# Kernel tuning notes

Hardware: AMD Instinct MI355X
Metric: run time of the kernel (lower is better)

## Reference

```python
import jax, jax.numpy as jnp
import numpy as np
from jax import lax

# Mamba2 block (training path: mamba_split_conv1d_scan_combined equivalent)
B = 2; L = 2048; D_MODEL = 2048
INTER = 4096          # ssm_intermediate_size
NH = 64; HD = INTER // NH   # num_heads, head_dim
N = 128               # ssm_state_size
G = 1                 # n_groups
K = 4                 # conv kernel
CS = 256              # chunk size
EPS = 1e-5
CONV_DIM = INTER + 2 * G * N          # 4352
PROJ_DIM = INTER + CONV_DIM + NH      # 8512


def setup_inputs() -> dict:
    key = jax.random.key(0)
    ks = jax.random.split(key, 4)
    std = 0.02
    return {
        "hidden_states": jax.random.normal(ks[0], (B, L, D_MODEL), jnp.float32),
        "W_in": jax.random.normal(ks[1], (PROJ_DIM, D_MODEL), jnp.float32) * std,
        "conv_w": jax.random.normal(ks[2], (CONV_DIM, K), jnp.float32) * std,
        "conv_b": jnp.zeros((CONV_DIM,), jnp.float32),
        "dt_bias": jnp.ones((NH,), jnp.float32),
        "A_log": jnp.log(jnp.arange(1, NH + 1, dtype=jnp.float32)),
        "D": jnp.ones((NH,), jnp.float32),
        "norm_w": jnp.ones((INTER,), jnp.float32),
        "W_out": jax.random.normal(ks[3], (D_MODEL, INTER), jnp.float32) * std,
    }


def _segsum(x):
    # x: [..., s] -> [..., s, s] lower-triangular cumulative sums (masked with -inf)
    s = x.shape[-1]
    xc = jnp.cumsum(x, axis=-1)
    d = xc[..., :, None] - xc[..., None, :]
    return jnp.where(jnp.tril(jnp.ones((s, s), dtype=bool)), d, -jnp.inf)


def _forward(hidden_states, W_in, conv_w, conv_b, dt_bias, A_log, D, norm_w, W_out):
    proj = hidden_states @ W_in.T                              # [B,L,PROJ_DIM]
    gate = proj[..., :INTER]
    hBC = proj[..., INTER:INTER + CONV_DIM]
    dt = proj[..., INTER + CONV_DIM:]                          # [B,L,NH]

    # causal depthwise conv1d + silu
    xc = hBC.transpose(0, 2, 1)                                # [B,CONV_DIM,L]
    y = lax.conv_general_dilated(
        xc, conv_w[:, None, :], (1,), [(K - 1, 0)],
        dimension_numbers=("NCH", "OIH", "NCH"), feature_group_count=CONV_DIM)
    hBC = jax.nn.silu(y + conv_b[None, :, None]).transpose(0, 2, 1)

    x = hBC[..., :INTER].reshape(B, L, NH, HD)
    Bm = hBC[..., INTER:INTER + G * N].reshape(B, L, G, N)
    Cm = hBC[..., INTER + G * N:].reshape(B, L, G, N)

    dtv = jax.nn.softplus(dt + dt_bias)                        # [B,L,NH], dt_softplus=True
    A = -jnp.exp(A_log)                                        # [NH]

    # ---- chunked selective scan (SSD) ----
    c = L // CS
    xch = x.reshape(B, c, CS, NH, HD)
    dtch = dtv.reshape(B, c, CS, NH)
    Bh = jnp.repeat(Bm.reshape(B, c, CS, G, N), NH // G, axis=3)   # [B,c,s,NH,N]
    Ch = jnp.repeat(Cm.reshape(B, c, CS, G, N), NH // G, axis=3)

    dA = (dtch * A).transpose(0, 3, 1, 2)                      # [B,NH,c,s]
    Acum = jnp.cumsum(dA, axis=-1)                             # [B,NH,c,s]
    Lmat = jnp.exp(_segsum(dA))                                # [B,NH,c,s,s]

    # within-chunk (diagonal block) output
    Ydiag = jnp.einsum("bcihn,bcjhn,bhcij,bcjh,bcjhp->bcihp",
                       Ch, Bh, Lmat, dtch, xch)

    # per-chunk states
    decay_states = jnp.exp(Acum[..., -1:] - Acum)              # [B,NH,c,s]
    states = jnp.einsum("bcjhn,bhcj,bcjh,bcjhp->bchpn",
                        Bh, decay_states, dtch, xch)           # [B,c,NH,HD,N]

    # inter-chunk recurrence (scan over chunks)
    chunk_decay = jnp.exp(Acum[..., -1])                       # [B,NH,c]

    def step(carry, inp):
        st, dec = inp
        new = dec[:, :, None, None] * carry + st
        return new, carry                                      # emit state at chunk start

    init = jnp.zeros((B, NH, HD, N), dtype=x.dtype)
    _, prev = lax.scan(step, init,
                       (states.transpose(1, 0, 2, 3, 4), chunk_decay.transpose(2, 0, 1)))
    prev = prev.transpose(1, 0, 2, 3, 4)                       # [B,c,NH,HD,N]

    Yoff = jnp.einsum("bcihn,bchpn,bhci->bcihp", Ch, prev, jnp.exp(Acum))

    Y = (Ydiag + Yoff).reshape(B, L, NH, HD) + x * D[None, None, :, None]
    yout = Y.reshape(B, L, INTER)

    # gated RMSNorm (norm_before_gate=False): gate first, then normalize
    yout = yout * jax.nn.silu(gate)
    yout = yout * lax.rsqrt(jnp.mean(yout * yout, axis=-1, keepdims=True) + EPS) * norm_w
    return yout @ W_out.T                                      # [B,L,D_MODEL]


def reference(hidden_states, W_in, conv_w, conv_b, dt_bias, A_log, D, norm_w, W_out):
    return _forward(hidden_states, W_in, conv_w, conv_b, dt_bias, A_log, D, norm_w, W_out)
```

## Files before the change

kernel.cpp:

```cpp
#include <hip/hip_runtime.h>
#include <cstdint>

typedef __bf16 bf16;
typedef __bf16 bf16x8 __attribute__((ext_vector_type(8)));
typedef __bf16 bf16x4 __attribute__((ext_vector_type(4)));
typedef float  f32x4  __attribute__((ext_vector_type(4)));

#define BQ     2
#define LQ     2048
#define DMODEL 2048
#define INTER  4096
#define NH     64
#define HD     64
#define NS     128
#define CS     256
#define NC     8
#define CONVD  4352
#define PROJD  8512
#define PROJP  8576
#define MTOT   4096
#define EPSF   1e-5f
#define LOG2E  1.44269504088896f

__device__ __forceinline__ void async_ld16(const bf16* g, bf16* l) {
  __builtin_amdgcn_global_load_lds(
      (__attribute__((address_space(1))) void*)(uintptr_t)g,
      (__attribute__((address_space(3))) void*)l, 16, 0, 0);
}

__device__ __forceinline__ float siluf(float x) { return x / (1.f + expf(-x)); }

__global__ void cast4_k(const float* __restrict__ in, bf16* __restrict__ out, long n4) {
  long i = (long)blockIdx.x * 256 + threadIdx.x;
  if (i >= n4) return;
  float4 v = ((const float4*)in)[i];
  bf16x4 o; o[0] = (bf16)v.x; o[1] = (bf16)v.y; o[2] = (bf16)v.z; o[3] = (bf16)v.w;
  ((bf16x4*)out)[i] = o;
}

__global__ void cast_pad_win_k(const float* __restrict__ W, bf16* __restrict__ out) {
  long i = (long)blockIdx.x * 256 + threadIdx.x;
  long tot = (long)PROJP * (DMODEL / 4);
  if (i >= tot) return;
  long row = i / (DMODEL / 4);
  long k4  = i % (DMODEL / 4);
  bf16x4 o;
  if (row < PROJD) {
    float4 v = ((const float4*)W)[row * (DMODEL / 4) + k4];
    o[0] = (bf16)v.x; o[1] = (bf16)v.y; o[2] = (bf16)v.z; o[3] = (bf16)v.w;
  } else {
    o[0] = o[1] = o[2] = o[3] = (bf16)0.f;
  }
  ((bf16x4*)out)[i] = o;
}

#define BM 128
#define BN 128
#define BK 32

__global__ __launch_bounds__(256) void gemm_bt(
    const bf16* __restrict__ A, const bf16* __restrict__ W,
    bf16* __restrict__ Cb, float* __restrict__ Cf,
    int M, int Nn, int K, int outf32)
{
  __shared__ bf16 As[BM * BK];
  __shared__ bf16 Bs[BN * BK];
  const int tid  = threadIdx.x;
  const int wave = tid >> 6;
  const int lane = tid & 63;
  const long tm = (long)blockIdx.y * BM;
  const long tn = (long)blockIdx.x * BN;
  const int wm = (wave >> 1) * 64;
  const int wn = (wave & 1) * 64;
  const int quad = lane >> 4;
  const int r16  = lane & 15;

  f32x4 acc[4][4] = {};

  for (long k0 = 0; k0 < K; k0 += BK) {
    __syncthreads();
    #pragma unroll
    for (int p = 0; p < 2; ++p) {
      int row = p * 64 + (tid >> 2);
      int kc  = (tid & 3) * 8;
      async_ld16(A + (tm + row) * K + k0 + kc, &As[(p * 256 + wave * 64) * 8]);
      async_ld16(W + (tn + row) * K + k0 + kc, &Bs[(p * 256 + wave * 64) * 8]);
    }
    __syncthreads();
    bf16x8 af[4], bfr[4];
    #pragma unroll
    for (int i = 0; i < 4; ++i)
      af[i] = *(const bf16x8*)&As[(wm + i * 16 + r16) * BK + quad * 8];
    #pragma unroll
    for (int j = 0; j < 4; ++j)
      bfr[j] = *(const bf16x8*)&Bs[(wn + j * 16 + r16) * BK + quad * 8];
    #pragma unroll
    for (int i = 0; i < 4; ++i)
      #pragma unroll
      for (int j = 0; j < 4; ++j)
        acc[i][j] = __builtin_amdgcn_mfma_f32_16x16x32_bf16(af[i], bfr[j], acc[i][j], 0, 0, 0);
  }

  #pragma unroll
  for (int i = 0; i < 4; ++i)
    #pragma unroll
    for (int j = 0; j < 4; ++j) {
      long r0 = tm + wm + i * 16 + quad * 4;
      long cc = tn + wn + j * 16 + r16;
      #pragma unroll
      for (int reg = 0; reg < 4; ++reg) {
        long idx = (r0 + reg) * (long)Nn + cc;
        if (outf32) Cf[idx] = acc[i][j][reg];
        else        Cb[idx] = (bf16)acc[i][j][reg];
      }
    }
}

__global__ void conv_silu_k(const bf16* __restrict__ proj,
                            const float* __restrict__ conv_w,
                            const float* __restrict__ conv_b,
                            bf16* __restrict__ xconv,
                            bf16* __restrict__ Bmb, bf16* __restrict__ Cmb)
{
  int ch = blockIdx.x * 256 + threadIdx.x;
  if (ch >= CONVD) return;
  long bl = blockIdx.y;
  int l = (int)(bl & (LQ - 1));
  float acc = conv_b[ch];
  #pragma unroll
  for (int t = 0; t < 4; ++t) {
    int ls = l - 3 + t;
    if (ls >= 0)
      acc += (float)proj[(bl - 3 + t) * PROJP + INTER + ch] * conv_w[ch * 4 + t];
  }
  float y = siluf(acc);
  if (ch < INTER)            xconv[bl * INTER + ch] = (bf16)y;
  else if (ch < INTER + NS)  Bmb[bl * NS + (ch - INTER)] = (bf16)y;
  else                       Cmb[bl * NS + (ch - INTER - NS)] = (bf16)y;
}

__global__ __launch_bounds__(CS) void dt_prep_k(
    const bf16* __restrict__ proj, const float* __restrict__ dt_bias,
    const float* __restrict__ A_log,
    float* __restrict__ dtv, float* __restrict__ acum, float* __restrict__ cdec)
{
  int bx = blockIdx.x;
  int ci = bx & 7;
  int bh = bx >> 3;
  int h  = bh & 63;
  int b  = bh >> 6;
  int i  = threadIdx.x;
  long pos = (long)b * LQ + ci * CS + i;
  float draw = (float)proj[pos * PROJP + INTER + CONVD + h] + dt_bias[h];
  float dv = draw > 20.f ? draw : log1pf(expf(draw));
  float Ah = -expf(A_log[h]);
  __shared__ float s[CS];
  s[i] = dv * Ah;
  __syncthreads();
  for (int off = 1; off < CS; off <<= 1) {
    float t = (i >= off) ? s[i - off] : 0.f;
    __syncthreads();
    s[i] += t;
    __syncthreads();
  }
  long base = (long)bx * CS;
  dtv[base + i]  = dv;
  acum[base + i] = s[i];
  if (i == 0) cdec[bx] = expf(s[CS - 1]);
}

__global__ __launch_bounds__(256) void gmat_k(
    const bf16* __restrict__ Cmb, const bf16* __restrict__ Bmb, float* __restrict__ Gnt)
{
  int q  = blockIdx.x;
  int bc = blockIdx.y;
  long bl0 = (long)(bc >> 3) * LQ + (bc & 7) * CS;
  int wave = threadIdx.x >> 6, lane = threadIdx.x & 63;
  int quad = lane >> 4, r16 = lane & 15;
  int i0 = (q >> 1) * 128 + (wave >> 1) * 64;
  int j0 = (q & 1)  * 128 + (wave & 1)  * 64;

  f32x4 acc[4][4] = {};
  #pragma unroll
  for (int kt = 0; kt < 4; ++kt) {
    int k0 = kt * 32 + quad * 8;
    bf16x8 af[4], bfv[4];
    #pragma unroll
    for (int it = 0; it < 4; ++it)
      af[it] = *(const bf16x8*)&Cmb[(bl0 + i0 + it * 16 + r16) * NS + k0];
    #pragma unroll
    for (int nt = 0; nt < 4; ++nt)
      bfv[nt] = *(const bf16x8*)&Bmb[(bl0 + j0 + nt * 16 + r16) * NS + k0];
    #pragma unroll
    for (int it = 0; it < 4; ++it)
      #pragma unroll
      for (int nt = 0; nt < 4; ++nt)
        acc[it][nt] = __builtin_amdgcn_mfma_f32_16x16x32_bf16(af[it], bfv[nt], acc[it][nt], 0, 0, 0);
  }
  #pragma unroll
  for (int it = 0; it < 4; ++it)
    #pragma unroll
    for (int nt = 0; nt < 4; ++nt)
      #pragma unroll
      for (int reg = 0; reg < 4; ++reg) {
        int i = i0 + it * 16 + quad * 4 + reg;
        int j = j0 + nt * 16 + r16;
        Gnt[((long)bc * CS + i) * CS + j] = acc[it][nt][reg];
      }
}

__global__ __launch_bounds__(256) void states_k(
    const bf16* __restrict__ xconv, const bf16* __restrict__ Bmb,
    const float* __restrict__ dtv, const float* __restrict__ acum,
    bf16* __restrict__ states)
{
  int bx = blockIdx.x;
  int h = bx & 63, bc = bx >> 6;
  int b = bc >> 3, ci = bc & 7;
  long bl0 = (long)b * LQ + ci * CS;
  long abase = ((long)(b * NH + h) * NC + ci) * CS;
  int t = threadIdx.x;
  __shared__ float ac_s[CS];
  __shared__ float ws_s[CS];
  __shared__ float xw[64][64];
  __shared__ float Bl[64][NS];
  ac_s[t] = acum[abase + t];
  __syncthreads();
  float alast = ac_s[CS - 1];
  ws_s[t] = expf(alast - ac_s[t]) * dtv[abase + t];
  int p = t & 63, nb = t >> 6;
  float accv[32] = {};
  for (int jt = 0; jt < 4; ++jt) {
    __syncthreads();
    for (int r = 0; r < 16; ++r) {
      int jj = (t >> 6) + r * 4;
      xw[jj][p] = (float)xconv[(bl0 + jt * 64 + jj) * INTER + h * HD + p] * ws_s[jt * 64 + jj];
    }
    for (int r = 0; r < 32; ++r) {
      int idx = t + r * 256;
      int jj = idx >> 7, n = idx & 127;
      Bl[jj][n] = (float)Bmb[(bl0 + jt * 64 + jj) * NS + n];
    }
    __syncthreads();
    for (int jj = 0; jj < 64; ++jj) {
      float xv = xw[jj][p];
      #pragma unroll
      for (int n0 = 0; n0 < 32; ++n0)
        accv[n0] += xv * Bl[jj][nb * 32 + n0];
    }
  }
  long sb = ((long)bx * HD + p) * NS + nb * 32;
  #pragma unroll
  for (int n0 = 0; n0 < 32; ++n0) states[sb + n0] = (bf16)accv[n0];
}

__global__ void scan_k(bf16* __restrict__ st, const float* __restrict__ cdec)
{
  long t = (long)blockIdx.x * 256 + threadIdx.x;
  int n = (int)(t & 127);
  int p = (int)((t >> 7) & 63);
  int h = (int)((t >> 13) & 63);
  int b = (int)(t >> 19);
  float carry = 0.f;
  for (int ci = 0; ci < NC; ++ci) {
    long idx = (((long)(b * NC + ci) * NH + h) * HD + p) * NS + n;
    float v = (float)st[idx];
    st[idx] = (bf16)carry;
    carry = cdec[(b * NH + h) * NC + ci] * carry + v;
  }
}

#define XTP 392
__global__ __launch_bounds__(256) void ymix_k(
    const bf16* __restrict__ xconv, const float* __restrict__ Gnt,
    const bf16* __restrict__ prev, const bf16* __restrict__ Cmb,
    const float* __restrict__ dtv, const float* __restrict__ acum,
    const float* __restrict__ Dp, bf16* __restrict__ Y)
{
  int bx = blockIdx.x;
  int h = bx & 63, bc = bx >> 6;
  int b = bc >> 3, ci = bc & 7;
  long bl0 = (long)b * LQ + ci * CS;
  long abase = ((long)(b * NH + h) * NC + ci) * CS;
  int t = threadIdx.x;
  int wave = t >> 6, lane = t & 63;
  int quad = lane >> 4, r16 = lane & 15;
  int iw = wave * 64;

  __shared__ bf16 Xt[64][XTP];
  __shared__ float a2s[CS], dts[CS], eas[CS];

  {
    float ac = acum[abase + t];
    a2s[t] = ac * LOG2E;
    dts[t] = dtv[abase + t];
    eas[t] = expf(ac);
  }
  {
    int col = t & 63, grp = t >> 6;
    for (int r = 0; r < 64; ++r) {
      int j = grp * 64 + r;
      Xt[col][j] = xconv[(bl0 + j) * INTER + h * HD + col];
    }
  }
  for (int r = 0; r < 32; ++r) {
    int idx = t + r * 256;
    int n = idx & 127, p = idx >> 7;
    Xt[p][256 + n] = prev[((long)bx * HD + p) * NS + n];
  }
  __syncthreads();

  f32x4 acc[4][4] = {};

  for (int kt = 0; kt < 12; ++kt) {
    int k0 = kt * 32;
    bool cpart = (k0 >= 256);
    if (!cpart && k0 > iw + 63) continue;

    bf16x8 bfrag[4];
    #pragma unroll
    for (int nt = 0; nt < 4; ++nt)
      bfrag[nt] = *(const bf16x8*)&Xt[nt * 16 + r16][k0 + quad * 8];

    if (!cpart) {
      int j0 = k0 + quad * 8;
      float dt8[8], a28[8];
      *(float4*)&dt8[0] = *(const float4*)&dts[j0];
      *(float4*)&dt8[4] = *(const float4*)&dts[j0 + 4];
      *(float4*)&a28[0] = *(const float4*)&a2s[j0];
      *(float4*)&a28[4] = *(const float4*)&a2s[j0 + 4];
      #pragma unroll
      for (int it = 0; it < 4; ++it) {
        if (k0 > iw + it * 16 + 15) continue;
        int i = iw + it * 16 + r16;
        float a2i = a2s[i];
        const float* gp = &Gnt[((long)bc * CS + i) * CS + j0];
        float g[8];
        *(float4*)&g[0] = *(const float4*)gp;
        *(float4*)&g[4] = *(const float4*)(gp + 4);
        bf16x8 af;
        #pragma unroll
        for (int jj = 0; jj < 8; ++jj) {
          float v = g[jj] * dt8[jj] * exp2f(a2i - a28[jj]);
          v = (j0 + jj <= i) ? v : 0.f;
          af[jj] = (bf16)v;
        }
        #pragma unroll
        for (int nt = 0; nt < 4; ++nt)
          acc[it][nt] = __builtin_amdgcn_mfma_f32_16x16x32_bf16(af, bfrag[nt], acc[it][nt], 0, 0, 0);
      }
    } else {
      int n0 = k0 - 256 + quad * 8;
      #pragma unroll
      for (int it = 0; it < 4; ++it) {
        int i = iw + it * 16 + r16;
        float e = eas[i];
        bf16x8 cv = *(const bf16x8*)&Cmb[(bl0 + i) * NS + n0];
        bf16x8 af;
        #pragma unroll
        for (int jj = 0; jj < 8; ++jj)
          af[jj] = (bf16)(e * (float)cv[jj]);
        #pragma unroll
        for (int nt = 0; nt < 4; ++nt)
          acc[it][nt] = __builtin_amdgcn_mfma_f32_16x16x32_bf16(af, bfrag[nt], acc[it][nt], 0, 0, 0);
      }
    }
  }

  float Dh = Dp[h];
  #pragma unroll
  for (int it = 0; it < 4; ++it)
    #pragma unroll
    for (int nt = 0; nt < 4; ++nt) {
      int i0 = iw + it * 16 + quad * 4;
      int p  = nt * 16 + r16;
      bf16x4 xv = *(const bf16x4*)&Xt[p][i0];
      #pragma unroll
      for (int reg = 0; reg < 4; ++reg) {
        float v = acc[it][nt][reg] + Dh * (float)xv[reg];
        Y[(bl0 + i0 + reg) * INTER + h * HD + p] = (bf16)v;
      }
    }
}

__global__ __launch_bounds__(256) void norm_k(
    bf16* __restrict__ Y, const bf16* __restrict__ proj,
    const float* __restrict__ norm_w)
{
  long bl = blockIdx.x;
  int t = threadIdx.x;
  __shared__ float yb[INTER];
  __shared__ float red[256];
  float ss = 0.f;
  for (int r = 0; r < 16; ++r) {
    int ch = t + r * 256;
    float g = (float)proj[bl * PROJP + ch];
    float yv = (float)Y[bl * INTER + ch] * siluf(g);
    yb[ch] = yv;
    ss += yv * yv;
  }
  red[t] = ss;
  __syncthreads();
  for (int s = 128; s > 0; s >>= 1) {
    if (t < s) red[t] += red[t + s];
    __syncthreads();
  }
  float scale = rsqrtf(red[0] / (float)INTER + EPSF);
  for (int r = 0; r < 16; ++r) {
    int ch = t + r * 256;
    Y[bl * INTER + ch] = (bf16)(yb[ch] * scale * norm_w[ch]);
  }
}

extern "C" void kernel_launch(void* const* d_in, const int* in_sizes, int n_in,
                              void* d_out, int out_size, void* d_ws, size_t ws_size,
                              hipStream_t stream)
{
  (void)in_sizes; (void)n_in; (void)out_size; (void)ws_size;
  const float* hidden  = (const float*)d_in[0];
  const float* W_in    = (const float*)d_in[1];
  const float* conv_w  = (const float*)d_in[2];
  const float* conv_b  = (const float*)d_in[3];
  const float* dt_bias = (const float*)d_in[4];
  const float* A_log   = (const float*)d_in[5];
  const float* Dp      = (const float*)d_in[6];
  const float* norm_w  = (const float*)d_in[7];
  const float* W_out   = (const float*)d_in[8];
  float* out = (float*)d_out;

  char* ws    = (char*)d_ws;
  bf16* projb = (bf16*)(ws);
  char* base2 = ws + 70254592;
  bf16*  hb    = (bf16*)(base2);
  bf16*  winb  = (bf16*)(base2 + 16777216);
  bf16*  xconv = (bf16*)(base2);
  bf16*  st    = (bf16*)(base2 + 33554432);
  float* Gnt   = (float*)(base2 + 50331648);
  bf16*  Bmb   = (bf16*)(base2 + 54525952);
  bf16*  Cmb   = (bf16*)(base2 + 55574528);
  float* dtv   = (float*)(base2 + 56623104);
  float* acum  = (float*)(base2 + 57671680);
  float* cdec  = (float*)(base2 + 58720256);
  bf16*  Yb    = xconv;
  bf16*  woutb = st;

  cast4_k<<<dim3((unsigned)((MTOT * (long)DMODEL / 4 + 255) / 256)), 256, 0, stream>>>(
      hidden, hb, (long)MTOT * DMODEL / 4);
  cast_pad_win_k<<<dim3((unsigned)(((long)PROJP * (DMODEL / 4) + 255) / 256)), 256, 0, stream>>>(
      W_in, winb);
  gemm_bt<<<dim3(PROJP / BN, MTOT / BM), 256, 0, stream>>>(
      hb, winb, projb, nullptr, MTOT, PROJP, DMODEL, 0);

  conv_silu_k<<<dim3(CONVD / 256, MTOT), 256, 0, stream>>>(
      projb, conv_w, conv_b, xconv, Bmb, Cmb);
  dt_prep_k<<<dim3(BQ * NH * NC), CS, 0, stream>>>(
      projb, dt_bias, A_log, dtv, acum, cdec);
  gmat_k<<<dim3(4, BQ * NC), 256, 0, stream>>>(Cmb, Bmb, Gnt);
  states_k<<<dim3(BQ * NC * NH), 256, 0, stream>>>(xconv, Bmb, dtv, acum, st);
  scan_k<<<dim3(BQ * NH * HD * NS / 256), 256, 0, stream>>>(st, cdec);
  ymix_k<<<dim3(BQ * NC * NH), 256, 0, stream>>>(
      xconv, Gnt, st, Cmb, dtv, acum, Dp, Yb);

  cast4_k<<<dim3((unsigned)((DMODEL * (long)INTER / 4 + 255) / 256)), 256, 0, stream>>>(
      W_out, woutb, (long)DMODEL * INTER / 4);
  norm_k<<<dim3(MTOT), 256, 0, stream>>>(Yb, projb, norm_w);
  gemm_bt<<<dim3(DMODEL / BN, MTOT / BM), 256, 0, stream>>>(
      Yb, woutb, nullptr, out, MTOT, DMODEL, INTER, 1);
}
```

Baseline: 802.4 us.

## Use MFMA for chunk state computation and swizzle GEMM block order

The per-chunk states kernel now uses bf16 MFMA instructions in place of scalar FP32 FMAs. To supply the B operand in k-contiguous form, the conv kernel also writes a per-chunk transposed copy of B, and x is staged transposed in LDS with the decay weights applied before the bf16 cast. The GEMM additionally remaps block indices into groups of 8 row tiles to improve L2 reuse. The tradeoffs are extra strided global writes for the B transpose and some extra rounding from casting the weighted x to bf16.

```diff
diff --git a/kernel.cpp b/kernel.cpp
--- a/kernel.cpp
+++ b/kernel.cpp
@@ -68,8 +68,19 @@
   const int tid  = threadIdx.x;
   const int wave = tid >> 6;
   const int lane = tid & 63;
-  const long tm = (long)blockIdx.y * BM;
-  const long tn = (long)blockIdx.x * BN;
+
+  int bxi, byi;
+  {
+    int b = blockIdx.y * gridDim.x + blockIdx.x;
+    if ((gridDim.y & 7) == 0) {
+      int gs = gridDim.x * 8;
+      int g = b / gs, r = b % gs;
+      byi = g * 8 + (r & 7);
+      bxi = r >> 3;
+    } else { bxi = blockIdx.x; byi = blockIdx.y; }
+  }
+  const long tm = (long)byi * BM;
+  const long tn = (long)bxi * BN;
   const int wm = (wave >> 1) * 64;
   const int wn = (wave & 1) * 64;
   const int quad = lane >> 4;
@@ -120,7 +131,8 @@
                             const float* __restrict__ conv_w,
                             const float* __restrict__ conv_b,
                             bf16* __restrict__ xconv,
-                            bf16* __restrict__ Bmb, bf16* __restrict__ Cmb)
+                            bf16* __restrict__ Bmb, bf16* __restrict__ Cmb,
+                            bf16* __restrict__ Bt)
 {
   int ch = blockIdx.x * 256 + threadIdx.x;
   if (ch >= CONVD) return;
@@ -134,9 +146,16 @@
       acc += (float)proj[(bl - 3 + t) * PROJP + INTER + ch] * conv_w[ch * 4 + t];
   }
   float y = siluf(acc);
-  if (ch < INTER)            xconv[bl * INTER + ch] = (bf16)y;
-  else if (ch < INTER + NS)  Bmb[bl * NS + (ch - INTER)] = (bf16)y;
-  else                       Cmb[bl * NS + (ch - INTER - NS)] = (bf16)y;
+  if (ch < INTER) {
+    xconv[bl * INTER + ch] = (bf16)y;
+  } else if (ch < INTER + NS) {
+    int n = ch - INTER;
+    Bmb[bl * NS + n] = (bf16)y;
+    int b = (int)(bl >> 11), ci = l >> 8, j = l & 255;
+    Bt[(((long)(b * NC + ci) * NS) + n) * CS + j] = (bf16)y;
+  } else {
+    Cmb[bl * NS + (ch - INTER - NS)] = (bf16)y;
+  }
 }
 
 __global__ __launch_bounds__(CS) void dt_prep_k(
@@ -210,9 +229,9 @@
 }
 
 __global__ __launch_bounds__(256) void states_k(
-    const bf16* __restrict__ xconv, const bf16* __restrict__ Bmb,
+    const bf16* __restrict__ xconv, const bf16* __restrict__ Bt,
     const float* __restrict__ dtv, const float* __restrict__ acum,
-    bf16* __restrict__ states)
+    bf16* __restrict__ st)
 {
   int bx = blockIdx.x;
   int h = bx & 63, bc = bx >> 6;
@@ -220,38 +239,51 @@
   long bl0 = (long)b * LQ + ci * CS;
   long abase = ((long)(b * NH + h) * NC + ci) * CS;
   int t = threadIdx.x;
+  int wave = t >> 6, lane = t & 63, quad = lane >> 4, r16 = lane & 15;
+
+  __shared__ bf16 Xt[64][264];
+  __shared__ float ws[CS];
   __shared__ float ac_s[CS];
-  __shared__ float ws_s[CS];
-  __shared__ float xw[64][64];
-  __shared__ float Bl[64][NS];
   ac_s[t] = acum[abase + t];
   __syncthreads();
   float alast = ac_s[CS - 1];
-  ws_s[t] = expf(alast - ac_s[t]) * dtv[abase + t];
-  int p = t & 63, nb = t >> 6;
-  float accv[32] = {};
-  for (int jt = 0; jt < 4; ++jt) {
-    __syncthreads();
-    for (int r = 0; r < 16; ++r) {
-      int jj = (t >> 6) + r * 4;
-      xw[jj][p] = (float)xconv[(bl0 + jt * 64 + jj) * INTER + h * HD + p] * ws_s[jt * 64 + jj];
-    }
-    for (int r = 0; r < 32; ++r) {
-      int idx = t + r * 256;
-      int jj = idx >> 7, n = idx & 127;
-      Bl[jj][n] = (float)Bmb[(bl0 + jt * 64 + jj) * NS + n];
-    }
-    __syncthreads();
-    for (int jj = 0; jj < 64; ++jj) {
-      float xv = xw[jj][p];
-      #pragma unroll
-      for (int n0 = 0; n0 < 32; ++n0)
-        accv[n0] += xv * Bl[jj][nb * 32 + n0];
-    }
-  }
-  long sb = ((long)bx * HD + p) * NS + nb * 32;
-  #pragma unroll
-  for (int n0 = 0; n0 < 32; ++n0) states[sb + n0] = (bf16)accv[n0];
+  ws[t] = expf(alast - ac_s[t]) * dtv[abase + t];
+  {
+    int col = t & 63, grp = t >> 6;
+    for (int r = 0; r < 64; ++r) {
+      int j = grp * 64 + r;
+      Xt[col][j] = xconv[(bl0 + j) * INTER + h * HD + col];
+    }
+  }
+  __syncthreads();
+
+  const bf16* btb = &Bt[(long)bc * NS * CS];
+  f32x4 acc[8] = {};
+  int p = wave * 16 + r16;
+  #pragma unroll
+  for (int kt = 0; kt < 8; ++kt) {
+    int k0 = kt * 32 + quad * 8;
+    bf16x8 xv = *(const bf16x8*)&Xt[p][k0];
+    float w8[8];
+    *(float4*)&w8[0] = *(const float4*)&ws[k0];
+    *(float4*)&w8[4] = *(const float4*)&ws[k0 + 4];
+    bf16x8 af;
+    #pragma unroll
+    for (int jj = 0; jj < 8; ++jj) af[jj] = (bf16)((float)xv[jj] * w8[jj]);
+    #pragma unroll
+    for (int nt = 0; nt < 8; ++nt) {
+      bf16x8 bfv = *(const bf16x8*)&btb[(nt * 16 + r16) * CS + k0];
+      acc[nt] = __builtin_amdgcn_mfma_f32_16x16x32_bf16(af, bfv, acc[nt], 0, 0, 0);
+    }
+  }
+  #pragma unroll
+  for (int nt = 0; nt < 8; ++nt)
+    #pragma unroll
+    for (int reg = 0; reg < 4; ++reg) {
+      int prow = wave * 16 + quad * 4 + reg;
+      int n = nt * 16 + r16;
+      st[((long)bx * HD + prow) * NS + n] = (bf16)acc[nt][reg];
+    }
 }
 
 __global__ void scan_k(bf16* __restrict__ st, const float* __restrict__ cdec)
@@ -441,6 +473,7 @@
   float* dtv   = (float*)(base2 + 56623104);
   float* acum  = (float*)(base2 + 57671680);
   float* cdec  = (float*)(base2 + 58720256);
+  bf16*  Bt    = (bf16*)(base2 + 58724352);
   bf16*  Yb    = xconv;
   bf16*  woutb = st;
 
@@ -452,11 +485,11 @@
       hb, winb, projb, nullptr, MTOT, PROJP, DMODEL, 0);
 
   conv_silu_k<<<dim3(CONVD / 256, MTOT), 256, 0, stream>>>(
-      projb, conv_w, conv_b, xconv, Bmb, Cmb);
+      projb, conv_w, conv_b, xconv, Bmb, Cmb, Bt);
   dt_prep_k<<<dim3(BQ * NH * NC), CS, 0, stream>>>(
       projb, dt_bias, A_log, dtv, acum, cdec);
   gmat_k<<<dim3(4, BQ * NC), 256, 0, stream>>>(Cmb, Bmb, Gnt);
-  states_k<<<dim3(BQ * NC * NH), 256, 0, stream>>>(xconv, Bmb, dtv, acum, st);
+  states_k<<<dim3(BQ * NC * NH), 256, 0, stream>>>(xconv, Bt, dtv, acum, st);
   scan_k<<<dim3(BQ * NH * HD * NS / 256), 256, 0, stream>>>(st, cdec);
   ymix_k<<<dim3(BQ * NC * NH), 256, 0, stream>>>(
       xconv, Gnt, st, Cmb, dtv, acum, Dp, Yb);
```

Result: faster. 705.4 us (-12.1%).
